# Kernel optimization log

Hardware: AMD Instinct MI355X
Metric: run time of the kernel (lower is better)

The kernel has to match this reference:

```python
import jax, jax.numpy as jnp
import numpy as np

B, S, D, H = 2, 2048, 1024, 16
HD = D // H  # 64


def setup_inputs() -> dict:
    key = jax.random.key(0)
    ks = jax.random.split(key, 11)
    w_scale = 1.0 / np.sqrt(D)
    Q = jax.random.normal(ks[0], (B, S, D), jnp.float32)
    K = jax.random.normal(ks[1], (B, S, D), jnp.float32)
    V = jax.random.normal(ks[2], (B, S, D), jnp.float32)
    # causal mask: True = masked (matches torch masked_fill semantics)
    mask = ~jnp.tril(jnp.ones((S, S), bool))[None, None]  # [1,1,S,S]
    # RoPE freqs (precomputed cos/sin of freqs_cis, shape [S, HD//2])
    inv_freq = 1.0 / (10000.0 ** (jnp.arange(0, HD, 2, dtype=jnp.float32) / HD))
    angles = jnp.arange(S, dtype=jnp.float32)[:, None] * inv_freq[None, :]
    freqs_cos, freqs_sin = jnp.cos(angles), jnp.sin(angles)
    wq = jax.random.normal(ks[3], (D, D), jnp.float32) * w_scale
    wk = jax.random.normal(ks[4], (D, D), jnp.float32) * w_scale
    wv = jax.random.normal(ks[5], (D, D), jnp.float32) * w_scale
    wo = jax.random.normal(ks[6], (D, D), jnp.float32) * w_scale
    bq = jax.random.normal(ks[7], (D,), jnp.float32) * 0.01
    bk = jax.random.normal(ks[8], (D,), jnp.float32) * 0.01
    bv = jax.random.normal(ks[9], (D,), jnp.float32) * 0.01
    bo = jax.random.normal(ks[10], (D,), jnp.float32) * 0.01
    return {"Q": Q, "K": K, "V": V, "mask": mask,
            "freqs_cos": freqs_cos, "freqs_sin": freqs_sin,
            "wq": wq, "bq": bq, "wk": wk, "bk": bk,
            "wv": wv, "bv": bv, "wo": wo, "bo": bo}


def _rope(x, cos, sin):
    # x: [B,S,H,HD]; complex pairing of adjacent dims as in view_as_complex
    xr, xi = x[..., 0::2], x[..., 1::2]
    c = cos[None, :, None, :]
    s = sin[None, :, None, :]
    out_r = xr * c - xi * s
    out_i = xr * s + xi * c
    return jnp.stack([out_r, out_i], axis=-1).reshape(x.shape)


def reference(Q, K, V, mask, freqs_cos, freqs_sin, wq, bq, wk, bk, wv, bv, wo, bo):
    b, s, d = Q.shape
    h = H
    hd = d // h
    q = (Q @ wq.T + bq).reshape(b, s, h, hd)
    k = (K @ wk.T + bk).reshape(b, s, h, hd)
    v = (V @ wv.T + bv).reshape(b, s, h, hd)
    q = _rope(q, freqs_cos, freqs_sin)
    k = _rope(k, freqs_cos, freqs_sin)
    q = q.transpose(0, 2, 1, 3)  # [B,H,S,HD]
    k = k.transpose(0, 2, 1, 3)
    v = v.transpose(0, 2, 1, 3)
    scale = jnp.sqrt(jnp.float32(hd))
    energy = jnp.einsum('bhqd,bhkd->bhqk', q, k) / scale
    energy = jnp.where(mask, jnp.float32(-1e10), energy)
    attn = jax.nn.softmax(energy, axis=-1)  # dropout p=0.0 -> identity
    out = jnp.einsum('bhqk,bhkd->bhqd', attn, v)
    out = out.transpose(0, 2, 1, 3).reshape(b, s, d)
    return out @ wo.T + bo
```

## Files before the change

kernel.cpp:

```cpp
#include <hip/hip_runtime.h>
#include <stdint.h>

#define NB 2
#define NS 2048
#define ND 1024
#define NH 16
#define NHD 64
#define NM (NB*NS)

typedef __bf16 bf16;
typedef float f32x4 __attribute__((ext_vector_type(4)));
typedef __bf16 bf16x8 __attribute__((ext_vector_type(8)));
typedef __bf16 bf16x4 __attribute__((ext_vector_type(4)));

#define MFMA16(a,b,c) __builtin_amdgcn_mfma_f32_16x16x32_bf16(a,b,c,0,0,0)

__device__ __forceinline__ void gld_lds16(const bf16* g, bf16* l) {
  __builtin_amdgcn_global_load_lds((const __attribute__((address_space(1))) void*)g,
                                   (__attribute__((address_space(3))) void*)l,
                                   16, 0, 0);
}

__device__ __forceinline__ void block_sync_lds() {
  asm volatile("s_waitcnt lgkmcnt(0)\n\ts_barrier" ::: "memory");
}

__global__ __launch_bounds__(256)
void cvt7(const float* __restrict__ s0, const float* __restrict__ s1,
          const float* __restrict__ s2, const float* __restrict__ s3,
          const float* __restrict__ s4, const float* __restrict__ s5,
          const float* __restrict__ s6, bf16* __restrict__ dst) {
  const int t = blockIdx.y;
  const float* s = (t == 0) ? s0 : (t == 1) ? s1 : (t == 2) ? s2 :
                   (t == 3) ? s3 : (t == 4) ? s4 : (t == 5) ? s5 : s6;
  const int n4 = (t < 3) ? (1 << 20) : (1 << 18);
  const size_t eoff = (t < 3) ? ((size_t)t << 22) : ((size_t)12 << 20) + ((size_t)(t - 3) << 20);
  int i = blockIdx.x * blockDim.x + threadIdx.x;
  if (i >= n4) return;
  float4 v = ((const float4*)s)[i];
  bf16x4 o = { (bf16)v.x, (bf16)v.y, (bf16)v.z, (bf16)v.w };
  ((bf16x4*)(dst + eoff))[i] = o;
}

template<int MODE>
__global__ __launch_bounds__(256)
void gemm_nt(const bf16* __restrict__ A, const bf16* __restrict__ W,
             const float* __restrict__ b0, const float* __restrict__ b1,
             const float* __restrict__ b2,
             const float* __restrict__ fc, const float* __restrict__ fs,
             bf16* __restrict__ obf, bf16* __restrict__ vtp,
             float* __restrict__ of) {
  constexpr int K = ND;
  constexpr int BN = (MODE == 0) ? 128 : 64;
  constexpr int NJ = (MODE == 0) ? 4 : 2;
  constexpr int ITB = (MODE == 0) ? 4 : 2;
  __shared__ __align__(16) bf16 As[128 * 64];
  __shared__ __align__(16) bf16 Bs[BN * 64];
  const int tid = threadIdx.x;
  const int w = tid >> 6, lane = tid & 63;

  const int id = blockIdx.x;
  const int xcd = id & 7, r = id >> 3;
  int t, nt, mt;
  if (MODE == 0) { t = r >> 5; const int rem = r & 31; nt = rem & 7;  mt = xcd + 8 * (rem >> 3); }
  else           { t = 0;                              nt = r & 15;   mt = xcd + 8 * (r >> 4);   }

  const bf16* Ab = A + (size_t)t * ((size_t)NM * K);
  const bf16* Wb = W + (size_t)t * ((size_t)ND * K);
  const float* bias = (t == 0) ? b0 : (t == 1) ? b1 : b2;
  const int wr = (w >> 1) * 64, wc = (w & 1) * (BN / 2);
  f32x4 acc[4][NJ] = {};

  const int swsrc = (((lane & 7) ^ ((lane >> 3) & 7)) << 3);
  const bf16* ga = Ab + (size_t)(mt * 128 + w * 8 + (lane >> 3)) * K + swsrc;
  const bf16* gb = Wb + (size_t)(nt * BN + w * 8 + (lane >> 3)) * K + swsrc;

  for (int k0 = 0; k0 < K; k0 += 64) {
    __syncthreads();
#pragma unroll
    for (int it = 0; it < 4; ++it)
      gld_lds16(ga + (size_t)(it * 32) * K + k0, As + (it * 4 + w) * 512);
#pragma unroll
    for (int it = 0; it < ITB; ++it)
      gld_lds16(gb + (size_t)(it * 32) * K + k0, Bs + (it * 4 + w) * 512);
    __syncthreads();

#pragma unroll
    for (int ks = 0; ks < 2; ++ks) {
      bf16x8 af[4], bfr[NJ];
#pragma unroll
      for (int i = 0; i < 4; ++i) {
        const int row = wr + i * 16 + (lane & 15);
        af[i] = *(const bf16x8*)&As[row * 64 +
                 (((ks * 4 + (lane >> 4)) ^ (lane & 7)) << 3)];
      }
#pragma unroll
      for (int j = 0; j < NJ; ++j) {
        const int row = wc + j * 16 + (lane & 15);
        bfr[j] = *(const bf16x8*)&Bs[row * 64 +
                  (((ks * 4 + (lane >> 4)) ^ (lane & 7)) << 3)];
      }
#pragma unroll
      for (int i = 0; i < 4; ++i)
#pragma unroll
        for (int j = 0; j < NJ; ++j)
          acc[i][j] = MFMA16(af[i], bfr[j], acc[i][j]);
    }
  }

#pragma unroll
  for (int i = 0; i < 4; ++i) {
#pragma unroll
    for (int j = 0; j < NJ; ++j) {
      const int gcol = nt * BN + wc + j * 16 + (lane & 15);
      const float bv = bias[gcol];
      if (MODE == 0 && t == 2) {
        const int s0g = mt * 128 + wr + i * 16 + (lane >> 4) * 4;
        const int b = s0g >> 11, s = s0g & (NS - 1);
        const int h = gcol >> 6, hd = gcol & 63;
        bf16x4 pk = { (bf16)(acc[i][j][0] + bv), (bf16)(acc[i][j][1] + bv),
                      (bf16)(acc[i][j][2] + bv), (bf16)(acc[i][j][3] + bv) };
        *(bf16x4*)&vtp[((size_t)(b * NH + h) * NHD + hd) * NS + s] = pk;
        continue;
      }
#pragma unroll
      for (int r4 = 0; r4 < 4; ++r4) {
        const int grow = mt * 128 + wr + i * 16 + (lane >> 4) * 4 + r4;
        float v = acc[i][j][r4] + bv;
        if (MODE == 0) {
          const int b = grow >> 11, s = grow & (NS - 1);
          const int h = gcol >> 6, hd = gcol & 63;
          float pv = __shfl_xor(v, 1);
          const int ii = hd >> 1;
          float c  = fc[(s << 5) + ii];
          float sn = fs[(s << 5) + ii];
          v = ((hd & 1) == 0) ? (v * c - pv * sn) : (pv * sn + v * c);
          if (t == 0) v *= 0.18033688011112042f;
          obf[(size_t)t * ((size_t)NM * ND) +
              (((size_t)(b * NH + h) * NS + s) * NHD + hd)] = (bf16)v;
        } else {
          of[(size_t)grow * ND + gcol] = v;
        }
      }
    }
  }
}

__device__ __forceinline__ void attn_tile(
    const bf16* __restrict__ Ksh, const bf16* __restrict__ Vsh,
    bf16* __restrict__ Pw, const bf16x8* qf, f32x4* o,
    float& m, float& l, int qi, int kk0, bool diag, int qrow, int grp) {
  const int s7 = qrow & 7;
  f32x4 sc[4] = {};
  __builtin_amdgcn_s_setprio(1);
#pragma unroll
  for (int ch = 0; ch < 2; ++ch)
#pragma unroll
    for (int cb = 0; cb < 4; ++cb) {
      bf16x8 kf = *(const bf16x8*)
        &Ksh[(cb * 16 + qrow) * 64 + (((ch * 4 + grp) ^ s7) << 3)];
      sc[cb] = MFMA16(kf, qf[ch], sc[cb]);
    }
  __builtin_amdgcn_s_setprio(0);

  if (diag) {
#pragma unroll
    for (int cb = 0; cb < 4; ++cb)
#pragma unroll
      for (int r = 0; r < 4; ++r)
        if (kk0 + cb * 16 + grp * 4 + r > qi) sc[cb][r] = -1e30f;
  }

  float a0 = fmaxf(fmaxf(sc[0][0], sc[0][1]), fmaxf(sc[0][2], sc[0][3]));
  float a1 = fmaxf(fmaxf(sc[1][0], sc[1][1]), fmaxf(sc[1][2], sc[1][3]));
  float a2 = fmaxf(fmaxf(sc[2][0], sc[2][1]), fmaxf(sc[2][2], sc[2][3]));
  float a3 = fmaxf(fmaxf(sc[3][0], sc[3][1]), fmaxf(sc[3][2], sc[3][3]));
  float pm = fmaxf(fmaxf(a0, a1), fmaxf(a2, a3));

  if (__any(pm > m + 8.f)) {
    float px = fmaxf(pm, __shfl_xor(pm, 16));
    px = fmaxf(px, __shfl_xor(px, 32));
    const float mn = fmaxf(m, px);
    const float scl = exp2f(m - mn);
    m = mn;
    l *= scl;
#pragma unroll
    for (int hb = 0; hb < 4; ++hb)
#pragma unroll
      for (int r = 0; r < 4; ++r) o[hb][r] *= scl;
  }

#pragma unroll
  for (int cb = 0; cb < 4; ++cb) {
    bf16x4 pk;
#pragma unroll
    for (int r = 0; r < 4; ++r) {
      float p = exp2f(sc[cb][r] - m);
      l += p;
      pk[r] = (bf16)p;
    }
    *(bf16x4*)&Pw[qrow * 64 + (((((cb << 1) | (grp >> 1)) ^ s7) << 3)) +
                  ((grp & 1) << 2)] = pk;
  }

  __builtin_amdgcn_s_setprio(1);
#pragma unroll
  for (int ch = 0; ch < 2; ++ch) {
    bf16x8 pa = *(const bf16x8*)
      &Pw[qrow * 64 + (((ch * 4 + grp) ^ s7) << 3)];
#pragma unroll
    for (int hb = 0; hb < 4; ++hb) {
      bf16x8 vf = *(const bf16x8*)
        &Vsh[(hb * 16 + qrow) * 64 + (((ch * 4 + grp) ^ s7) << 3)];
      o[hb] = MFMA16(vf, pa, o[hb]);
    }
  }
  __builtin_amdgcn_s_setprio(0);
}

__global__ __launch_bounds__(512, 4)
void attn_k(const bf16* __restrict__ q, const bf16* __restrict__ k,
            const bf16* __restrict__ vt, bf16* __restrict__ out) {
  __shared__ __align__(16) char smem[81920];
  bf16* KV = (bf16*)smem;
  bf16* Pr = (bf16*)(smem + 65536);
  auto MO = (float(*)[2][16][68])smem;
  auto ML = (float(*)[2][16][2])(smem + 36864);

  const int tid = threadIdx.x;
  const int w = tid >> 6, lane = tid & 63;
  const int h = w >> 2, wl = w & 3;
  const int qrow = lane & 15, grp = lane >> 4;
  const int bh = blockIdx.x, j = blockIdx.y;
  const int b = bh >> 4, hh = bh & (NH - 1);
  const int tA = j, tB = 31 - j;

  const bf16* qb = q + (size_t)bh * NS * NHD;
  const bf16* kb = k + (size_t)bh * NS * NHD;
  const bf16* vb = vt + (size_t)bh * NHD * NS;

  const int nA = (j >= h) ? (((j - h) >> 1) + 1) : 0;
  const int nB = (((31 - j) - h) >> 1) + 1;
  const int len = nA + nB;

  const int q0A = tA * 64 + wl * 16, q0B = tB * 64 + wl * 16;
  bf16x8 qfA[2], qfB[2];
#pragma unroll
  for (int ch = 0; ch < 2; ++ch) {
    qfA[ch] = *(const bf16x8*)&qb[(size_t)(q0A + qrow) * NHD + ch * 32 + grp * 8];
    qfB[ch] = *(const bf16x8*)&qb[(size_t)(q0B + qrow) * NHD + ch * 32 + grp * 8];
  }

  f32x4 oA[4] = {}, oB[4] = {};
  float mA = -1e30f, lA = 0.f, mB = -1e30f, lB = 0.f;

  const int local = tid & 255;
  const int r0 = local >> 3;
  const int c0 = (local & 7) * 8;
  const int sw = (((local & 7) ^ (r0 & 7)) << 3);

  bf16* Pw = Pr + w * 1024;
  auto Kb = [&](int buf) { return KV + ((h * 2 + buf) * 2 + 0) * 4096; };
  auto Vb = [&](int buf) { return KV + ((h * 2 + buf) * 2 + 1) * 4096; };

  bf16x8 ka0, ka1, va0, va1;
  auto load_round = [&](int r) {
    const bool isA = r < nA;
    const int kt = isA ? (h + 2 * r) : (h + 2 * (r - nA));
    const int kk0 = kt * 64;
    ka0 = *(const bf16x8*)&kb[(size_t)(kk0 + r0) * NHD + c0];
    ka1 = *(const bf16x8*)&kb[(size_t)(kk0 + r0 + 32) * NHD + c0];
    va0 = *(const bf16x8*)&vb[(size_t)r0 * NS + kk0 + c0];
    va1 = *(const bf16x8*)&vb[(size_t)(r0 + 32) * NS + kk0 + c0];
  };
  auto store_tile = [&](int buf) {
    bf16* Ksc = Kb(buf);
    bf16* Vsc = Vb(buf);
    *(bf16x8*)&Ksc[r0 * 64 + sw]        = ka0;
    *(bf16x8*)&Ksc[(r0 + 32) * 64 + sw] = ka1;
    *(bf16x8*)&Vsc[r0 * 64 + sw]        = va0;
    *(bf16x8*)&Vsc[(r0 + 32) * 64 + sw] = va1;
  };

  load_round(0);
  store_tile(0);
  load_round(1);
  block_sync_lds();

  for (int r = 0; r < 17; ++r) {
    const int cur = r & 1;
    const bool act = r < len;
    if (r + 1 < len) store_tile(cur ^ 1);
    if (r + 2 < len) load_round(r + 2);
    if (act) {
      const bool isA = r < nA;
      const int kt = isA ? (h + 2 * r) : (h + 2 * (r - nA));
      if (isA)
        attn_tile(Kb(cur), Vb(cur), Pw, qfA, oA, mA, lA,
                  q0A + qrow, kt * 64, kt == tA, qrow, grp);
      else
        attn_tile(Kb(cur), Vb(cur), Pw, qfB, oB, mB, lB,
                  q0B + qrow, kt * 64, kt == tB, qrow, grp);
    }
    block_sync_lds();
  }

  lA += __shfl_xor(lA, 16); lA += __shfl_xor(lA, 32);
  lB += __shfl_xor(lB, 16); lB += __shfl_xor(lB, 32);

  __syncthreads();

  if (h == 1) {
#pragma unroll
    for (int hb = 0; hb < 4; ++hb) {
      *(f32x4*)&MO[wl][0][qrow][hb * 16 + grp * 4] = oA[hb];
      *(f32x4*)&MO[wl][1][qrow][hb * 16 + grp * 4] = oB[hb];
    }
    if (grp == 0) {
      ML[wl][0][qrow][0] = mA; ML[wl][0][qrow][1] = lA;
      ML[wl][1][qrow][0] = mB; ML[wl][1][qrow][1] = lB;
    }
  }
  __syncthreads();

  if (h == 0) {
#pragma unroll
    for (int sub = 0; sub < 2; ++sub) {
      const float m0 = sub ? mB : mA, l0 = sub ? lB : lA;
      const f32x4* o0 = sub ? oB : oA;
      const float m1 = ML[wl][sub][qrow][0], l1 = ML[wl][sub][qrow][1];
      const float mm = fmaxf(m0, m1);
      const float s0 = exp2f(m0 - mm), s1 = exp2f(m1 - mm);
      const float inv = 1.f / (l0 * s0 + l1 * s1);
      const int s = (sub ? q0B : q0A) + qrow;
      bf16* op = out + (size_t)(b * NS + s) * ND + hh * NHD + grp * 4;
#pragma unroll
      for (int hb = 0; hb < 4; ++hb) {
        f32x4 o1 = *(const f32x4*)&MO[wl][sub][qrow][hb * 16 + grp * 4];
        bf16x4 ov = { (bf16)((o0[hb][0] * s0 + o1[0] * s1) * inv),
                      (bf16)((o0[hb][1] * s0 + o1[1] * s1) * inv),
                      (bf16)((o0[hb][2] * s0 + o1[2] * s1) * inv),
                      (bf16)((o0[hb][3] * s0 + o1[3] * s1) * inv) };
        *(bf16x4*)&op[hb * 16] = ov;
      }
    }
  }
}

extern "C" void kernel_launch(void* const* d_in, const int* in_sizes, int n_in,
                              void* d_out, int out_size, void* d_ws, size_t ws_size,
                              hipStream_t stream) {
  const float* Q  = (const float*)d_in[0];
  const float* K  = (const float*)d_in[1];
  const float* V  = (const float*)d_in[2];
  const float* fc = (const float*)d_in[4];
  const float* fs = (const float*)d_in[5];
  const float* wq = (const float*)d_in[6];
  const float* bq = (const float*)d_in[7];
  const float* wk = (const float*)d_in[8];
  const float* bk = (const float*)d_in[9];
  const float* wv = (const float*)d_in[10];
  const float* bv = (const float*)d_in[11];
  const float* wo = (const float*)d_in[12];
  const float* bo = (const float*)d_in[13];
  float* out = (float*)d_out;
  bf16* ws = (bf16*)d_ws;

  const size_t MB_ = 1024 * 1024;
  bf16* Qbf  = ws;
  bf16* Wqkv = ws + 12 * MB_;
  bf16* Wo   = ws + 15 * MB_;
  bf16* qp   = ws + 16 * MB_;
  bf16* kp   = ws + 20 * MB_;
  bf16* vtp  = ws + 28 * MB_;
  bf16* aout = ws + 32 * MB_;

  cvt7<<<dim3(4096, 7), 256, 0, stream>>>(Q, K, V, wq, wk, wv, wo, ws);

  gemm_nt<0><<<768, 256, 0, stream>>>(Qbf, Wqkv, bq, bk, bv, fc, fs,
                                      qp, vtp, nullptr);

  attn_k<<<dim3(32, 16), 512, 0, stream>>>(qp, kp, vtp, aout);

  gemm_nt<1><<<512, 256, 0, stream>>>(aout, Wo, bo, bo, bo, fc, fs,
                                      nullptr, nullptr, out);
}
```

Baseline: 122.0 us.

## Share K/V tiles between paired query tiles in attention; shrink QKV GEMM tile

The attention kernel previously streamed K/V tiles for query tile A and then separately for tile B. Because A's key range is a prefix of B's, each loaded K/V tile is now used for both query tiles at once (dual QK MFMAs and two softmax/PV passes). This roughly halves the K/V global loads and rounds per block. Separately, the QKV projection GEMM drops from 128-wide to 64-wide N tiles, doubling the grid to 1536 blocks for better occupancy and load balance, at the cost of more A-tile reloads.

```diff
diff --git a/kernel.cpp b/kernel.cpp
--- a/kernel.cpp
+++ b/kernel.cpp
@@ -51,9 +51,9 @@
              bf16* __restrict__ obf, bf16* __restrict__ vtp,
              float* __restrict__ of) {
   constexpr int K = ND;
-  constexpr int BN = (MODE == 0) ? 128 : 64;
-  constexpr int NJ = (MODE == 0) ? 4 : 2;
-  constexpr int ITB = (MODE == 0) ? 4 : 2;
+  constexpr int BN = 64;
+  constexpr int NJ = 2;
+  constexpr int ITB = 2;
   __shared__ __align__(16) bf16 As[128 * 64];
   __shared__ __align__(16) bf16 Bs[BN * 64];
   const int tid = threadIdx.x;
@@ -62,13 +62,13 @@
   const int id = blockIdx.x;
   const int xcd = id & 7, r = id >> 3;
   int t, nt, mt;
-  if (MODE == 0) { t = r >> 5; const int rem = r & 31; nt = rem & 7;  mt = xcd + 8 * (rem >> 3); }
+  if (MODE == 0) { t = r >> 6; const int rem = r & 63; nt = rem & 15; mt = xcd + 8 * (rem >> 4); }
   else           { t = 0;                              nt = r & 15;   mt = xcd + 8 * (r >> 4);   }
 
   const bf16* Ab = A + (size_t)t * ((size_t)NM * K);
   const bf16* Wb = W + (size_t)t * ((size_t)ND * K);
   const float* bias = (t == 0) ? b0 : (t == 1) ? b1 : b2;
-  const int wr = (w >> 1) * 64, wc = (w & 1) * (BN / 2);
+  const int wr = (w >> 1) * 64, wc = (w & 1) * 32;
   f32x4 acc[4][NJ] = {};
 
   const int swsrc = (((lane & 7) ^ ((lane >> 3) & 7)) << 3);
@@ -146,31 +146,18 @@
   }
 }
 
-__device__ __forceinline__ void attn_tile(
-    const bf16* __restrict__ Ksh, const bf16* __restrict__ Vsh,
-    bf16* __restrict__ Pw, const bf16x8* qf, f32x4* o,
-    float& m, float& l, int qi, int kk0, bool diag, int qrow, int grp) {
+__device__ __forceinline__ void mask_diag(f32x4* sc, int qi, int kk0, int grp) {
+#pragma unroll
+  for (int cb = 0; cb < 4; ++cb)
+#pragma unroll
+    for (int r = 0; r < 4; ++r)
+      if (kk0 + cb * 16 + grp * 4 + r > qi) sc[cb][r] = -1e30f;
+}
+
+__device__ __forceinline__ void softmax_pv(
+    f32x4* sc, bf16* __restrict__ Pw, const bf16* __restrict__ Vsh,
+    f32x4* o, float& m, float& l, int qrow, int grp) {
   const int s7 = qrow & 7;
-  f32x4 sc[4] = {};
-  __builtin_amdgcn_s_setprio(1);
-#pragma unroll
-  for (int ch = 0; ch < 2; ++ch)
-#pragma unroll
-    for (int cb = 0; cb < 4; ++cb) {
-      bf16x8 kf = *(const bf16x8*)
-        &Ksh[(cb * 16 + qrow) * 64 + (((ch * 4 + grp) ^ s7) << 3)];
-      sc[cb] = MFMA16(kf, qf[ch], sc[cb]);
-    }
-  __builtin_amdgcn_s_setprio(0);
-
-  if (diag) {
-#pragma unroll
-    for (int cb = 0; cb < 4; ++cb)
-#pragma unroll
-      for (int r = 0; r < 4; ++r)
-        if (kk0 + cb * 16 + grp * 4 + r > qi) sc[cb][r] = -1e30f;
-  }
-
   float a0 = fmaxf(fmaxf(sc[0][0], sc[0][1]), fmaxf(sc[0][2], sc[0][3]));
   float a1 = fmaxf(fmaxf(sc[1][0], sc[1][1]), fmaxf(sc[1][2], sc[1][3]));
   float a2 = fmaxf(fmaxf(sc[2][0], sc[2][1]), fmaxf(sc[2][2], sc[2][3]));
@@ -206,8 +193,7 @@
   __builtin_amdgcn_s_setprio(1);
 #pragma unroll
   for (int ch = 0; ch < 2; ++ch) {
-    bf16x8 pa = *(const bf16x8*)
-      &Pw[qrow * 64 + (((ch * 4 + grp) ^ s7) << 3)];
+    bf16x8 pa = *(const bf16x8*)&Pw[qrow * 64 + (((ch * 4 + grp) ^ s7) << 3)];
 #pragma unroll
     for (int hb = 0; hb < 4; ++hb) {
       bf16x8 vf = *(const bf16x8*)
@@ -241,7 +227,6 @@
 
   const int nA = (j >= h) ? (((j - h) >> 1) + 1) : 0;
   const int nB = (((31 - j) - h) >> 1) + 1;
-  const int len = nA + nB;
 
   const int q0A = tA * 64 + wl * 16, q0B = tB * 64 + wl * 16;
   bf16x8 qfA[2], qfB[2];
@@ -265,9 +250,7 @@
 
   bf16x8 ka0, ka1, va0, va1;
   auto load_round = [&](int r) {
-    const bool isA = r < nA;
-    const int kt = isA ? (h + 2 * r) : (h + 2 * (r - nA));
-    const int kk0 = kt * 64;
+    const int kk0 = (h + 2 * r) * 64;
     ka0 = *(const bf16x8*)&kb[(size_t)(kk0 + r0) * NHD + c0];
     ka1 = *(const bf16x8*)&kb[(size_t)(kk0 + r0 + 32) * NHD + c0];
     va0 = *(const bf16x8*)&vb[(size_t)r0 * NS + kk0 + c0];
@@ -287,20 +270,48 @@
   load_round(1);
   block_sync_lds();
 
-  for (int r = 0; r < 17; ++r) {
+  for (int r = 0; r < 16; ++r) {
     const int cur = r & 1;
-    const bool act = r < len;
-    if (r + 1 < len) store_tile(cur ^ 1);
-    if (r + 2 < len) load_round(r + 2);
+    const bool act = r < nB;
+    if (r + 1 < nB) store_tile(cur ^ 1);
+    if (r + 2 < nB) load_round(r + 2);
     if (act) {
-      const bool isA = r < nA;
-      const int kt = isA ? (h + 2 * r) : (h + 2 * (r - nA));
-      if (isA)
-        attn_tile(Kb(cur), Vb(cur), Pw, qfA, oA, mA, lA,
-                  q0A + qrow, kt * 64, kt == tA, qrow, grp);
-      else
-        attn_tile(Kb(cur), Vb(cur), Pw, qfB, oB, mB, lB,
-                  q0B + qrow, kt * 64, kt == tB, qrow, grp);
+      const int kt = h + 2 * r;
+      const int kk0 = kt * 64;
+      const bool dual = (r < nA);
+      const int s7 = qrow & 7;
+      const bf16* Ksh = Kb(cur);
+      if (dual) {
+        f32x4 sB[4] = {}, sA[4] = {};
+        __builtin_amdgcn_s_setprio(1);
+#pragma unroll
+        for (int ch = 0; ch < 2; ++ch)
+#pragma unroll
+          for (int cb = 0; cb < 4; ++cb) {
+            bf16x8 kf = *(const bf16x8*)
+              &Ksh[(cb * 16 + qrow) * 64 + (((ch * 4 + grp) ^ s7) << 3)];
+            sB[cb] = MFMA16(kf, qfB[ch], sB[cb]);
+            sA[cb] = MFMA16(kf, qfA[ch], sA[cb]);
+          }
+        __builtin_amdgcn_s_setprio(0);
+        if (kt == tA) mask_diag(sA, q0A + qrow, kk0, grp);
+        softmax_pv(sB, Pw, Vb(cur), oB, mB, lB, qrow, grp);
+        softmax_pv(sA, Pw, Vb(cur), oA, mA, lA, qrow, grp);
+      } else {
+        f32x4 sB[4] = {};
+        __builtin_amdgcn_s_setprio(1);
+#pragma unroll
+        for (int ch = 0; ch < 2; ++ch)
+#pragma unroll
+          for (int cb = 0; cb < 4; ++cb) {
+            bf16x8 kf = *(const bf16x8*)
+              &Ksh[(cb * 16 + qrow) * 64 + (((ch * 4 + grp) ^ s7) << 3)];
+            sB[cb] = MFMA16(kf, qfB[ch], sB[cb]);
+          }
+        __builtin_amdgcn_s_setprio(0);
+        if (kt == tB) mask_diag(sB, q0B + qrow, kk0, grp);
+        softmax_pv(sB, Pw, Vb(cur), oB, mB, lB, qrow, grp);
+      }
     }
     block_sync_lds();
   }
@@ -377,8 +388,8 @@
 
   cvt7<<<dim3(4096, 7), 256, 0, stream>>>(Q, K, V, wq, wk, wv, wo, ws);
 
-  gemm_nt<0><<<768, 256, 0, stream>>>(Qbf, Wqkv, bq, bk, bv, fc, fs,
-                                      qp, vtp, nullptr);
+  gemm_nt<0><<<1536, 256, 0, stream>>>(Qbf, Wqkv, bq, bk, bv, fc, fs,
+                                       qp, vtp, nullptr);
 
   attn_k<<<dim3(32, 16), 512, 0, stream>>>(qp, kp, vtp, aout);
 
```

New measurement: 123.5 us. No clear change (+1.2%).
